# Performance work log

Measured on AMD Instinct MI355X. Metric: run time of the kernel, lower is better.

Reference implementation:

```python
import jax, jax.numpy as jnp
import numpy as np

B, N, D = 16, 2048, 1024
H, DH = 8, 64
I = H * DH            # 512
L = 64                # num_latents
DEPTH = 6
FF = 4 * D


def setup_inputs() -> dict:
    key = jax.random.key(0)
    ks = jax.random.split(key, 8)
    s = 0.02  # weight scale to keep activations well-conditioned
    return {
        "x": jax.random.normal(ks[0], (B, N, D), jnp.float32),
        "mask": jax.random.randint(ks[1], (B, N), 0, 2, jnp.int32),
        "latents": jax.random.normal(ks[2], (L, D), jnp.float32),
        "ln_m_w": jnp.ones((DEPTH, D), jnp.float32),
        "ln_m_b": jnp.zeros((DEPTH, D), jnp.float32),
        "ln_l_w": jnp.ones((DEPTH, D), jnp.float32),
        "ln_l_b": jnp.zeros((DEPTH, D), jnp.float32),
        "Wq": jax.random.normal(ks[3], (DEPTH, D, I), jnp.float32) * s,
        "Wkv": jax.random.normal(ks[4], (DEPTH, D, 2 * I), jnp.float32) * s,
        "Wo": jax.random.normal(ks[5], (DEPTH, I, D), jnp.float32) * s,
        "ff_ln_w": jnp.ones((DEPTH, D), jnp.float32),
        "ff_ln_b": jnp.zeros((DEPTH, D), jnp.float32),
        "W1": jax.random.normal(ks[6], (DEPTH, D, FF), jnp.float32) * s,
        "W2": jax.random.normal(ks[7], (DEPTH, FF, D), jnp.float32) * s,
        "norm_w": jnp.ones((D,), jnp.float32),
        "norm_b": jnp.zeros((D,), jnp.float32),
    }


def _ln(x, w, b, eps=1e-5):
    mu = x.mean(-1, keepdims=True)
    var = ((x - mu) ** 2).mean(-1, keepdims=True)
    return (x - mu) * jax.lax.rsqrt(var + eps) * w + b


def reference(x, mask, latents, ln_m_w, ln_m_b, ln_l_w, ln_l_b,
              Wq, Wkv, Wo, ff_ln_w, ff_ln_b, W1, W2, norm_w, norm_b):
    b, n, d = x.shape
    Lq = latents.shape[0]
    depth = Wq.shape[0]
    h = H
    dh = Wq.shape[-1] // h
    scale = dh ** -0.5

    x4 = x[:, None]  # b 1 n d  (t = 1 media frame)
    lat = jnp.broadcast_to(latents, (b, 1, Lq, d)).astype(x.dtype)
    # mask==1 means masked-out; latents (L zeros) are always attendable
    fmask = jnp.concatenate([mask, jnp.zeros((b, Lq), mask.dtype)], axis=-1)
    mbool = (fmask == 1)[:, None, None, None, :]  # b 1 1 1 S -> broadcast to b t h i S

    for i in range(depth):
        xn = _ln(x4, ln_m_w[i], ln_m_b[i])
        lnl = _ln(lat, ln_l_w[i], ln_l_b[i])
        q = (lnl @ Wq[i]).reshape(b, 1, Lq, h, dh)
        kv = jnp.concatenate([xn, lnl], axis=-2) @ Wkv[i]  # b 1 S 2I
        k, v = jnp.split(kv, 2, axis=-1)
        S = k.shape[-2]
        k = k.reshape(b, 1, S, h, dh)
        v = v.reshape(b, 1, S, h, dh)
        sim = jnp.einsum('btihd,btjhd->bthij', q, k) * scale
        sim = jnp.where(mbool, -jnp.inf, sim)
        sim = sim - jax.lax.stop_gradient(sim.max(axis=-1, keepdims=True))
        attn = jax.nn.softmax(sim, axis=-1)
        out = jnp.einsum('bthij,btjhd->btihd', attn, v).reshape(b, 1, Lq, h * dh)
        lat = out @ Wo[i] + lat
        hf = jax.nn.gelu(_ln(lat, ff_ln_w[i], ff_ln_b[i]) @ W1[i], approximate=False)
        lat = hf @ W2[i] + lat
    return _ln(lat, norm_w, norm_b)
```

## Files before the change

### kernel.cpp

```cpp
#include <hip/hip_runtime.h>

typedef unsigned short u16;
typedef unsigned int u32;
typedef __attribute__((ext_vector_type(8))) short short8;
typedef __attribute__((ext_vector_type(4))) float f4;

#define DEV static __device__ __forceinline__

constexpr int BB = 16, NN = 2048, DD = 1024, HH = 8, DHD = 64, II = 512, LL = 64, DEPTHC = 6, FFC = 4096;

DEV u16 f2bf(float f) {
  union { float f; u32 u; } v; v.f = f;
  u32 r = v.u + 0x7FFFu + ((v.u >> 16) & 1u);
  return (u16)(r >> 16);
}

DEV u32 pack2(float lo, float hi) {
  return (u32)f2bf(lo) | ((u32)f2bf(hi) << 16);
}

typedef const u32 __attribute__((address_space(1)))* gas_p;
typedef u32 __attribute__((address_space(3)))* las_p;
DEV void gl_lds16(const void* g, void* l) {
  __builtin_amdgcn_global_load_lds((gas_p)g, (las_p)l, 16, 0, 0);
}

__global__ __launch_bounds__(256) void maskscan_k(const int* __restrict__ mask,
    int* __restrict__ idx, int* __restrict__ cnt) {
  int b = blockIdx.x, tid = threadIdx.x;
  int lane = tid & 63, wv = tid >> 6;
  const int* mrow = mask + (size_t)b * NN;
  int base = tid * 8;
  int keep[8]; int local = 0;
  #pragma unroll
  for (int j = 0; j < 8; j++) { keep[j] = (mrow[base + j] == 0); local += keep[j]; }
  int incl = local;
  #pragma unroll
  for (int off = 1; off < 64; off <<= 1) {
    int v = __shfl_up(incl, off, 64);
    if (lane >= off) incl += v;
  }
  __shared__ int wsum[4];
  if (lane == 63) wsum[wv] = incl;
  __syncthreads();
  int wbase = 0;
  for (int w = 0; w < wv; w++) wbase += wsum[w];
  int pos = wbase + incl - local;
  #pragma unroll
  for (int j = 0; j < 8; j++) if (keep[j]) idx[(size_t)b * NN + pos++] = base + j;
  if (tid == 255) cnt[b] = wbase + incl;
}

__global__ __launch_bounds__(256) void ln_gather_k(const float* __restrict__ x,
    const int* __restrict__ idx, const int* __restrict__ cnt, u16* __restrict__ xcomp) {
  int b = blockIdx.y, j = blockIdx.x, tid = threadIdx.x;
  int c = cnt[b];
  if (j >= ((c + 127) & ~127)) return;
  ushort4* orow = (ushort4*)(xcomp + ((size_t)b * NN + j) * DD);
  if (j >= c) { orow[tid] = make_ushort4(0, 0, 0, 0); return; }
  int src = idx[(size_t)b * NN + j];
  const float4* rp = (const float4*)(x + ((size_t)b * NN + src) * DD);
  float4 v = rp[tid];
  float s = v.x + v.y + v.z + v.w;
  float s2 = v.x*v.x + v.y*v.y + v.z*v.z + v.w*v.w;
  #pragma unroll
  for (int off = 32; off >= 1; off >>= 1) {
    s  += __shfl_xor(s, off, 64);
    s2 += __shfl_xor(s2, off, 64);
  }
  __shared__ float red[8];
  int wv = tid >> 6;
  if ((tid & 63) == 0) { red[wv] = s; red[4 + wv] = s2; }
  __syncthreads();
  s  = red[0] + red[1] + red[2] + red[3];
  s2 = red[4] + red[5] + red[6] + red[7];
  float mu = s * (1.f / DD);
  float var = s2 * (1.f / DD) - mu * mu;
  float rstd = rsqrtf(var + 1e-5f);
  orow[tid] = make_ushort4(f2bf((v.x - mu) * rstd), f2bf((v.y - mu) * rstd),
                           f2bf((v.z - mu) * rstd), f2bf((v.w - mu) * rstd));
}

template<bool OUTF32>
__global__ __launch_bounds__(256) void ln_rows_k(const float* __restrict__ in,
    const float* __restrict__ w, const float* __restrict__ bias, void* __restrict__ out) {
  int row = blockIdx.x;
  int tid = threadIdx.x;
  const float4* rp = (const float4*)(in + (size_t)row * DD);
  float4 x = rp[tid];
  float s = x.x + x.y + x.z + x.w;
  float s2 = x.x*x.x + x.y*x.y + x.z*x.z + x.w*x.w;
  #pragma unroll
  for (int off = 32; off >= 1; off >>= 1) {
    s  += __shfl_xor(s, off, 64);
    s2 += __shfl_xor(s2, off, 64);
  }
  __shared__ float red[8];
  int wv = tid >> 6;
  if ((tid & 63) == 0) { red[wv] = s; red[4 + wv] = s2; }
  __syncthreads();
  s  = red[0] + red[1] + red[2] + red[3];
  s2 = red[4] + red[5] + red[6] + red[7];
  float mu = s * (1.f / DD);
  float var = s2 * (1.f / DD) - mu * mu;
  float rstd = rsqrtf(var + 1e-5f);
  float y[4] = {x.x, x.y, x.z, x.w};
  int col = tid * 4;
  #pragma unroll
  for (int j = 0; j < 4; j++)
    y[j] = (y[j] - mu) * rstd * w[col + j] + bias[col + j];
  if (OUTF32) {
    float4 o = {y[0], y[1], y[2], y[3]};
    ((float4*)out)[(size_t)row * (DD/4) + tid] = o;
  } else {
    ushort4 o = make_ushort4(f2bf(y[0]), f2bf(y[1]), f2bf(y[2]), f2bf(y[3]));
    ((ushort4*)out)[(size_t)row * (DD/4) + tid] = o;
  }
}

__global__ __launch_bounds__(256) void lat_init_k(const float* __restrict__ latents, float* __restrict__ lat) {
  int idx = blockIdx.x * 256 + threadIdx.x;
  ((float4*)lat)[idx] = ((const float4*)latents)[idx & (LL * DD / 4 - 1)];
}

__global__ void zero_k(float* __restrict__ p, int n) {
  int i = blockIdx.x * 256 + threadIdx.x;
  if (i < n) p[i] = 0.f;
}

__global__ __launch_bounds__(256) void transpall_k(const float* __restrict__ WqA, const float* __restrict__ WkvA,
    const float* __restrict__ WoA, const float* __restrict__ W1A, const float* __restrict__ W2A,
    const float* __restrict__ lnwA, const float* __restrict__ lnbA,
    u16* __restrict__ WqkvTA, u16* __restrict__ WkvTfA, u16* __restrict__ WoTA,
    u16* __restrict__ W1TA, u16* __restrict__ W2TA, float* __restrict__ biaskvA) {
  __shared__ float t[64][65];
  int gid = blockIdx.x;
  int depth = gid / 2560;
  int id = gid % 2560;
  const float* in; u16* o1; int R, C, c0, r0;
  bool iskv = false;
  if (id < 128)       { in = WqA  + (size_t)depth*1024*512;  R = 1024; C = 512;  int l = id;        c0 = (l & 7) * 64;  r0 = (l >> 3) * 64; o1 = WqkvTA + (size_t)depth*1536*1024; }
  else if (id < 384)  { in = WkvA + (size_t)depth*1024*1024; R = 1024; C = 1024; int l = id - 128;  c0 = (l & 15) * 64; r0 = (l >> 4) * 64; o1 = WqkvTA + (size_t)depth*1536*1024 + 512*1024; iskv = true; }
  else if (id < 512)  { in = WoA  + (size_t)depth*512*1024;  R = 512;  C = 1024; int l = id - 384;  c0 = (l & 15) * 64; r0 = (l >> 4) * 64; o1 = WoTA + (size_t)depth*1024*512; }
  else if (id < 1536) { in = W1A  + (size_t)depth*1024*4096; R = 1024; C = 4096; int l = id - 512;  c0 = (l & 63) * 64; r0 = (l >> 6) * 64; o1 = W1TA + (size_t)depth*4096*1024; }
  else                { in = W2A  + (size_t)depth*4096*1024; R = 4096; C = 1024; int l = id - 1536; c0 = (l & 15) * 64; r0 = (l >> 4) * 64; o1 = W2TA + (size_t)depth*1024*4096; }
  int tid = threadIdx.x;
  int lr = tid >> 4, lc4 = (tid & 15) * 4;
  #pragma unroll
  for (int p = 0; p < 4; p++) {
    int row = p * 16 + lr;
    float4 v = *(const float4*)&in[(size_t)(r0 + row) * C + c0 + lc4];
    t[row][lc4] = v.x; t[row][lc4+1] = v.y; t[row][lc4+2] = v.z; t[row][lc4+3] = v.w;
  }
  int oc = tid >> 3;
  int rg = tid & 7;
  float lw[8], lb[8];
  if (iskv) {
    const float* lnw = lnwA + depth * 1024;
    const float* lnb = lnbA + depth * 1024;
    int rbase = r0 + rg * 8;
    float4 w0 = *(const float4*)&lnw[rbase];
    float4 w1 = *(const float4*)&lnw[rbase + 4];
    float4 b0 = *(const float4*)&lnb[rbase];
    float4 b1 = *(const float4*)&lnb[rbase + 4];
    lw[0]=w0.x; lw[1]=w0.y; lw[2]=w0.z; lw[3]=w0.w; lw[4]=w1.x; lw[5]=w1.y; lw[6]=w1.z; lw[7]=w1.w;
    lb[0]=b0.x; lb[1]=b0.y; lb[2]=b0.z; lb[3]=b0.w; lb[4]=b1.x; lb[5]=b1.y; lb[6]=b1.z; lb[7]=b1.w;
  }
  __syncthreads();
  #pragma unroll
  for (int p = 0; p < 2; p++) {
    int c = p * 32 + oc;
    float v[8];
    #pragma unroll
    for (int k = 0; k < 8; k++) v[k] = t[rg * 8 + k][c];
    int4 o;
    o.x = (int)pack2(v[0], v[1]); o.y = (int)pack2(v[2], v[3]);
    o.z = (int)pack2(v[4], v[5]); o.w = (int)pack2(v[6], v[7]);
    *(int4*)&o1[(size_t)(c0 + c) * R + r0 + rg * 8] = o;
    if (iskv) {
      u16* WkvTf = WkvTfA + (size_t)depth*1024*1024;
      int4 of;
      of.x = (int)pack2(v[0]*lw[0], v[1]*lw[1]); of.y = (int)pack2(v[2]*lw[2], v[3]*lw[3]);
      of.z = (int)pack2(v[4]*lw[4], v[5]*lw[5]); of.w = (int)pack2(v[6]*lw[6], v[7]*lw[7]);
      *(int4*)&WkvTf[(size_t)(c0 + c) * 1024 + r0 + rg * 8] = of;
      float partial = 0.f;
      #pragma unroll
      for (int k = 0; k < 8; k++) partial += lb[k] * v[k];
      partial += __shfl_xor(partial, 1, 64);
      partial += __shfl_xor(partial, 2, 64);
      partial += __shfl_xor(partial, 4, 64);
      if (rg == 0) atomicAdd(&biaskvA[depth*1024 + c0 + c], partial);
    }
  }
}

__global__ __launch_bounds__(256) void gemm_fused_k(
    const u16* __restrict__ xcomp, const u16* __restrict__ WkvTf,
    u16* __restrict__ kvk, u16* __restrict__ vT,
    const float* __restrict__ bias, const int* __restrict__ cnt,
    const u16* __restrict__ lnl, const u16* __restrict__ WqkvT, u16* __restrict__ qkv) {
  __shared__ __align__(16) u16 As[128 * 32];
  __shared__ __align__(16) u16 Bs[128 * 32];
  int id = blockIdx.x;
  int tid = threadIdx.x;
  int wv = tid >> 6, lane = tid & 63;
  const u16 *A, *B;
  int m0, n0, batch = 0, ml = 0;
  bool iskv;
  if (id < 2048) {
    int xg = id & 7, t = id >> 3;
    int mtile = xg * 32 + (t >> 3);
    n0 = (t & 7) * 128;
    batch = mtile >> 4;
    ml = (mtile & 15) * 128;
    if (ml >= cnt[batch]) return;
    m0 = batch * NN + ml;
    A = xcomp; B = WkvTf; iskv = true;
  } else {
    int l = id - 2048;
    m0 = (l / 12) * 128; n0 = (l % 12) * 128;
    A = lnl; B = WqkvT; iskv = false;
  }
  const int K = 1024;
  int srow = wv * 16 + (lane >> 2);
  int scol = (lane & 3) * 8;
  const u16* gA0 = A + (size_t)(m0 + srow) * K + scol;
  const u16* gA1 = A + (size_t)(m0 + 64 + srow) * K + scol;
  const u16* gB0 = B + (size_t)(n0 + srow) * K + scol;
  const u16* gB1 = B + (size_t)(n0 + 64 + srow) * K + scol;
  u16* lA0 = &As[srow * 32 + scol];
  u16* lA1 = &As[(64 + srow) * 32 + scol];
  u16* lB0 = &Bs[srow * 32 + scol];
  u16* lB1 = &Bs[(64 + srow) * 32 + scol];
  int wm = (wv & 1) * 64, wn = (wv >> 1) * 64;
  int fr = lane & 15, fq = (lane >> 4) * 8;
  f4 acc[4][4];
  #pragma unroll
  for (int mi = 0; mi < 4; mi++)
    #pragma unroll
    for (int ni = 0; ni < 4; ni++) acc[mi][ni] = f4{0.f, 0.f, 0.f, 0.f};

  for (int k0 = 0; k0 < K; k0 += 32) {
    gl_lds16(gA0 + k0, lA0);
    gl_lds16(gA1 + k0, lA1);
    gl_lds16(gB0 + k0, lB0);
    gl_lds16(gB1 + k0, lB1);
    __syncthreads();
    short8 af[4], bfr[4];
    #pragma unroll
    for (int mi = 0; mi < 4; mi++)
      af[mi] = *(const short8*)&As[(wm + mi*16 + fr) * 32 + fq];
    #pragma unroll
    for (int ni = 0; ni < 4; ni++)
      bfr[ni] = *(const short8*)&Bs[(wn + ni*16 + fr) * 32 + fq];
    #pragma unroll
    for (int mi = 0; mi < 4; mi++)
      #pragma unroll
      for (int ni = 0; ni < 4; ni++)
        acc[mi][ni] = __builtin_amdgcn_mfma_f32_16x16x32_bf16(af[mi], bfr[ni], acc[mi][ni], 0, 0, 0);
    __syncthreads();
  }
  int er = (lane >> 4) * 4;
  int ec = lane & 15;
  if (iskv) {
    #pragma unroll
    for (int mi = 0; mi < 4; mi++) {
      int rbase = wm + mi*16 + er;
      #pragma unroll
      for (int ni = 0; ni < 4; ni++) {
        int col = n0 + wn + ni*16 + ec;
        float bv = bias[col];
        if (col < 512) {
          #pragma unroll
          for (int r = 0; r < 4; r++)
            kvk[(size_t)(m0 + rbase + r) * 512 + col] = f2bf(acc[mi][ni][r] + bv);
        } else {
          int d = col - 512;
          int hh = d >> 6, dl = d & 63;
          ushort4 o4;
          o4.x = f2bf(acc[mi][ni][0] + bv);
          o4.y = f2bf(acc[mi][ni][1] + bv);
          o4.z = f2bf(acc[mi][ni][2] + bv);
          o4.w = f2bf(acc[mi][ni][3] + bv);
          *(ushort4*)(vT + ((size_t)((batch * 8 + hh) * 64 + dl)) * NN + (ml + rbase)) = o4;
        }
      }
    }
  } else {
    #pragma unroll
    for (int mi = 0; mi < 4; mi++)
      #pragma unroll
      for (int ni = 0; ni < 4; ni++) {
        int col = n0 + wn + ni*16 + ec;
        #pragma unroll
        for (int r = 0; r < 4; r++) {
          int row = m0 + wm + mi*16 + er + r;
          qkv[(size_t)row * 1536 + col] = f2bf(acc[mi][ni][r]);
        }
      }
  }
}

__global__ __launch_bounds__(256) void gemm_gelu_k(const u16* __restrict__ A, const u16* __restrict__ Bm,
    u16* __restrict__ C, int M, int N, int K) {
  __shared__ __align__(16) u16 As[128 * 32];
  __shared__ __align__(16) u16 Bs[64 * 32];
  int tid = threadIdx.x;
  int wv = tid >> 6, lane = tid & 63;
  int m0 = blockIdx.y * 128, n0 = blockIdx.x * 64;
  int srow = wv * 16 + (lane >> 2);
  int scol = (lane & 3) * 8;
  const u16* gA0 = A + (size_t)(m0 + srow) * K + scol;
  const u16* gA1 = A + (size_t)(m0 + 64 + srow) * K + scol;
  const u16* gB0 = Bm + (size_t)(n0 + srow) * K + scol;
  u16* lA0 = &As[srow * 32 + scol];
  u16* lA1 = &As[(64 + srow) * 32 + scol];
  u16* lB0 = &Bs[srow * 32 + scol];
  int wm = (wv & 1) * 64, wn = (wv >> 1) * 32;
  int fr = lane & 15, fq = (lane >> 4) * 8;
  f4 acc[4][2];
  #pragma unroll
  for (int mi = 0; mi < 4; mi++)
    #pragma unroll
    for (int ni = 0; ni < 2; ni++) acc[mi][ni] = f4{0.f, 0.f, 0.f, 0.f};

  for (int k0 = 0; k0 < K; k0 += 32) {
    gl_lds16(gA0 + k0, lA0);
    gl_lds16(gA1 + k0, lA1);
    gl_lds16(gB0 + k0, lB0);
    __syncthreads();
    short8 af[4], bfr[2];
    #pragma unroll
    for (int mi = 0; mi < 4; mi++)
      af[mi] = *(const short8*)&As[(wm + mi*16 + fr) * 32 + fq];
    #pragma unroll
    for (int ni = 0; ni < 2; ni++)
      bfr[ni] = *(const short8*)&Bs[(wn + ni*16 + fr) * 32 + fq];
    #pragma unroll
    for (int mi = 0; mi < 4; mi++)
      #pragma unroll
      for (int ni = 0; ni < 2; ni++)
        acc[mi][ni] = __builtin_amdgcn_mfma_f32_16x16x32_bf16(af[mi], bfr[ni], acc[mi][ni], 0, 0, 0);
    __syncthreads();
  }
  int er = (lane >> 4) * 4;
  int ec = lane & 15;
  #pragma unroll
  for (int mi = 0; mi < 4; mi++)
    #pragma unroll
    for (int ni = 0; ni < 2; ni++) {
      int col = n0 + wn + ni*16 + ec;
      #pragma unroll
      for (int r = 0; r < 4; r++) {
        int row = m0 + wm + mi*16 + er + r;
        float v = acc[mi][ni][r];
        v = 0.5f * v * (1.f + erff(v * 0.70710678118654752f));
        C[(size_t)row * N + col] = f2bf(v);
      }
    }
}

__global__ __launch_bounds__(256) void gemmsk_k(const u16* __restrict__ A, const u16* __restrict__ Bm,
    float* __restrict__ C, int M, int N, int K, int Kc) {
  __shared__ __align__(16) u16 As[128 * 32];
  __shared__ __align__(16) u16 Bs[64 * 32];
  int tid = threadIdx.x;
  int wv = tid >> 6, lane = tid & 63;
  int m0 = blockIdx.y * 128, n0 = blockIdx.x * 64;
  int kb = blockIdx.z * Kc;
  int srow = wv * 16 + (lane >> 2);
  int scol = (lane & 3) * 8;
  const u16* gA0 = A + (size_t)(m0 + srow) * K + kb + scol;
  const u16* gA1 = A + (size_t)(m0 + 64 + srow) * K + kb + scol;
  const u16* gB0 = Bm + (size_t)(n0 + srow) * K + kb + scol;
  u16* lA0 = &As[srow * 32 + scol];
  u16* lA1 = &As[(64 + srow) * 32 + scol];
  u16* lB0 = &Bs[srow * 32 + scol];
  int wm = (wv & 1) * 64, wn = (wv >> 1) * 32;
  int fr = lane & 15, fq = (lane >> 4) * 8;
  f4 acc[4][2];
  #pragma unroll
  for (int mi = 0; mi < 4; mi++)
    #pragma unroll
    for (int ni = 0; ni < 2; ni++) acc[mi][ni] = f4{0.f, 0.f, 0.f, 0.f};

  for (int k0 = 0; k0 < Kc; k0 += 32) {
    gl_lds16(gA0 + k0, lA0);
    gl_lds16(gA1 + k0, lA1);
    gl_lds16(gB0 + k0, lB0);
    __syncthreads();
    short8 af[4], bfr[2];
    #pragma unroll
    for (int mi = 0; mi < 4; mi++)
      af[mi] = *(const short8*)&As[(wm + mi*16 + fr) * 32 + fq];
    #pragma unroll
    for (int ni = 0; ni < 2; ni++)
      bfr[ni] = *(const short8*)&Bs[(wn + ni*16 + fr) * 32 + fq];
    #pragma unroll
    for (int mi = 0; mi < 4; mi++)
      #pragma unroll
      for (int ni = 0; ni < 2; ni++)
        acc[mi][ni] = __builtin_amdgcn_mfma_f32_16x16x32_bf16(af[mi], bfr[ni], acc[mi][ni], 0, 0, 0);
    __syncthreads();
  }
  int er = (lane >> 4) * 4;
  int ec = lane & 15;
  #pragma unroll
  for (int mi = 0; mi < 4; mi++)
    #pragma unroll
    for (int ni = 0; ni < 2; ni++) {
      int col = n0 + wn + ni*16 + ec;
      #pragma unroll
      for (int r = 0; r < 4; r++) {
        int row = m0 + wm + mi*16 + er + r;
        atomicAdd(&C[(size_t)row * N + col], acc[mi][ni][r]);
      }
    }
}

__global__ __launch_bounds__(256) void attn_part_k(const u16* __restrict__ qkv,
    const u16* __restrict__ kvk, const u16* __restrict__ vT, const int* __restrict__ cnt,
    float* __restrict__ opart, float* __restrict__ mlpart) {
  int id = blockIdx.x;
  int b = id >> 6;
  int h = (id >> 3) & 7;
  int part = id & 7;
  int tid = threadIdx.x;
  int wv = tid >> 6, lane = tid & 63;
  int fr = lane & 15, fq8 = (lane >> 4) * 8;
  int c = cnt[b];
  int nt = (c + 63) >> 6;
  int T = nt + 1;
  int t0 = (T * part) >> 3;
  int t1 = (T * (part + 1)) >> 3;

  __shared__ __align__(16) u16 ks[64 * 88];
  __shared__ __align__(16) u16 vs[64 * 88];
  __shared__ __align__(16) u16 ps[4][16 * 88];
  __shared__ float smask[64];

  const u16* qp = qkv + (size_t)(b * LL + wv * 16 + fr) * 1536 + h * DHD;
  short8 aq0 = *(const short8*)(qp + fq8);
  short8 aq1 = *(const short8*)(qp + 32 + fq8);

  float m_i[4], l_i[4];
  f4 o[4];
  #pragma unroll
  for (int r = 0; r < 4; r++) { m_i[r] = -1e30f; l_i[r] = 0.f; }
  #pragma unroll
  for (int dt = 0; dt < 4; dt++) o[dt] = f4{0.f, 0.f, 0.f, 0.f};

  const float scale = 0.125f;

  for (int t = t0; t < t1; t++) {
    bool isLat = (t == nt);
    __syncthreads();
    if (isLat) {
      const u16* src = qkv + (size_t)(b * LL) * 1536 + 512 + h * DHD;
      #pragma unroll
      for (int it = 0; it < 2; it++) {
        int cid = it * 256 + tid;
        int kr = cid >> 3, c8 = (cid & 7) * 8;
        int4 kvv = *(const int4*)(src + (size_t)kr * 1536 + c8);
        *(int4*)&ks[kr * 88 + c8] = kvv;
        int4 vvv = *(const int4*)(src + 512 + (size_t)kr * 1536 + c8);
        const u16* ve = (const u16*)&vvv;
        #pragma unroll
        for (int j = 0; j < 8; j++) vs[(c8 + j) * 88 + kr] = ve[j];
      }
    } else {
      const u16* ksrc = kvk + (size_t)(b * NN + t * 64) * 512 + h * DHD;
      const u16* vsrc = vT + (size_t)((b * 8 + h) * 64) * NN + t * 64;
      #pragma unroll
      for (int it = 0; it < 2; it++) {
        int cid = it * 256 + tid;
        int kr = cid >> 3, c8 = (cid & 7) * 8;
        *(int4*)&ks[kr * 88 + c8] = *(const int4*)(ksrc + (size_t)kr * 512 + c8);
        *(int4*)&vs[kr * 88 + c8] = *(const int4*)(vsrc + (size_t)kr * NN + c8);
      }
    }
    if (tid < 64)
      smask[tid] = (isLat || (t * 64 + tid < c)) ? 0.f : -1e30f;
    __syncthreads();

    f4 sim[4];
    #pragma unroll
    for (int ct = 0; ct < 4; ct++) {
      short8 b0 = *(const short8*)&ks[(ct*16 + fr) * 88 + fq8];
      short8 b1 = *(const short8*)&ks[(ct*16 + fr) * 88 + 32 + fq8];
      f4 s = f4{0.f, 0.f, 0.f, 0.f};
      s = __builtin_amdgcn_mfma_f32_16x16x32_bf16(aq0, b0, s, 0, 0, 0);
      s = __builtin_amdgcn_mfma_f32_16x16x32_bf16(aq1, b1, s, 0, 0, 0);
      float mk = smask[ct*16 + fr];
      #pragma unroll
      for (int r = 0; r < 4; r++) s[r] = s[r] * scale + mk;
      sim[ct] = s;
    }
    float mnew[4], alpha[4], p[4][4];
    #pragma unroll
    for (int r = 0; r < 4; r++) {
      float mx = fmaxf(fmaxf(sim[0][r], sim[1][r]), fmaxf(sim[2][r], sim[3][r]));
      #pragma unroll
      for (int off = 8; off >= 1; off >>= 1) mx = fmaxf(mx, __shfl_xor(mx, off, 16));
      mnew[r] = fmaxf(m_i[r], mx);
      alpha[r] = __expf(m_i[r] - mnew[r]);
      m_i[r] = mnew[r];
      float ssum = 0.f;
      #pragma unroll
      for (int ct = 0; ct < 4; ct++) { float e = __expf(sim[ct][r] - mnew[r]); p[ct][r] = e; ssum += e; }
      #pragma unroll
      for (int off = 8; off >= 1; off >>= 1) ssum += __shfl_xor(ssum, off, 16);
      l_i[r] = l_i[r] * alpha[r] + ssum;
    }
    #pragma unroll
    for (int ct = 0; ct < 4; ct++)
      #pragma unroll
      for (int r = 0; r < 4; r++)
        ps[wv][((lane>>4)*4 + r) * 88 + ct*16 + fr] = f2bf(p[ct][r]);
    #pragma unroll
    for (int dt = 0; dt < 4; dt++)
      #pragma unroll
      for (int r = 0; r < 4; r++) o[dt][r] *= alpha[r];
    short8 pa0 = *(const short8*)&ps[wv][fr * 88 + fq8];
    short8 pa1 = *(const short8*)&ps[wv][fr * 88 + 32 + fq8];
    #pragma unroll
    for (int dt = 0; dt < 4; dt++) {
      short8 bv0 = *(const short8*)&vs[(dt*16 + fr) * 88 + fq8];
      short8 bv1 = *(const short8*)&vs[(dt*16 + fr) * 88 + 32 + fq8];
      o[dt] = __builtin_amdgcn_mfma_f32_16x16x32_bf16(pa0, bv0, o[dt], 0, 0, 0);
      o[dt] = __builtin_amdgcn_mfma_f32_16x16x32_bf16(pa1, bv1, o[dt], 0, 0, 0);
    }
  }
  #pragma unroll
  for (int dt = 0; dt < 4; dt++)
    #pragma unroll
    for (int r = 0; r < 4; r++) {
      int row = wv * 16 + (lane>>4)*4 + r;
      int col = dt*16 + fr;
      opart[((size_t)id * 64 + row) * 64 + col] = o[dt][r];
    }
  if (fr == 0) {
    #pragma unroll
    for (int r = 0; r < 4; r++) {
      int row = wv * 16 + (lane>>4)*4 + r;
      mlpart[id * 128 + row * 2]     = m_i[r];
      mlpart[id * 128 + row * 2 + 1] = l_i[r];
    }
  }
}

__global__ __launch_bounds__(256) void attn_comb_k(const float* __restrict__ opart,
    const float* __restrict__ mlpart, u16* __restrict__ out) {
  int bh = blockIdx.x;
  int b = bh >> 3, h = bh & 7;
  int tid = threadIdx.x;
  int row = tid >> 2;
  int c0 = (tid & 3) * 16;
  float mp[8], lp[8];
  float m = -1e30f;
  #pragma unroll
  for (int p = 0; p < 8; p++) {
    mp[p] = mlpart[(bh * 8 + p) * 128 + row * 2];
    lp[p] = mlpart[(bh * 8 + p) * 128 + row * 2 + 1];
    m = fmaxf(m, mp[p]);
  }
  float a[8]; float L = 0.f;
  #pragma unroll
  for (int p = 0; p < 8; p++) { a[p] = __expf(mp[p] - m); L += lp[p] * a[p]; }
  float rl = 1.f / L;
  u16* op = out + ((size_t)(b * LL + row)) * II + h * DHD + c0;
  #pragma unroll
  for (int j = 0; j < 4; j++) {
    float acc4[4] = {0.f, 0.f, 0.f, 0.f};
    #pragma unroll
    for (int p = 0; p < 8; p++) {
      const float4* pp = (const float4*)(opart + ((size_t)(bh * 8 + p) * 64 + row) * 64 + c0);
      float4 v = pp[j];
      acc4[0] += v.x * a[p]; acc4[1] += v.y * a[p];
      acc4[2] += v.z * a[p]; acc4[3] += v.w * a[p];
    }
    op[j*4 + 0] = f2bf(acc4[0] * rl);
    op[j*4 + 1] = f2bf(acc4[1] * rl);
    op[j*4 + 2] = f2bf(acc4[2] * rl);
    op[j*4 + 3] = f2bf(acc4[3] * rl);
  }
}

extern "C" void kernel_launch(void* const* d_in, const int* in_sizes, int n_in,
                              void* d_out, int out_size, void* d_ws, size_t ws_size,
                              hipStream_t stream) {
  (void)in_sizes; (void)n_in; (void)out_size; (void)ws_size;
  const float* x       = (const float*)d_in[0];
  const int*   mask    = (const int*)d_in[1];
  const float* latents = (const float*)d_in[2];
  const float* ln_m_w  = (const float*)d_in[3];
  const float* ln_m_b  = (const float*)d_in[4];
  const float* ln_l_w  = (const float*)d_in[5];
  const float* ln_l_b  = (const float*)d_in[6];
  const float* Wq      = (const float*)d_in[7];
  const float* Wkv     = (const float*)d_in[8];
  const float* Wo      = (const float*)d_in[9];
  const float* ff_ln_w = (const float*)d_in[10];
  const float* ff_ln_b = (const float*)d_in[11];
  const float* W1      = (const float*)d_in[12];
  const float* W2      = (const float*)d_in[13];
  const float* norm_w  = (const float*)d_in[14];
  const float* norm_b  = (const float*)d_in[15];
  float* out = (float*)d_out;

  char* ws = (char*)d_ws;
  size_t off = 0;
  auto alloc = [&](size_t bytes) -> void* {
    void* p = ws + off; off += (bytes + 255) & ~(size_t)255; return p;
  };
  u16* xcomp = (u16*)alloc((size_t)32768 * 1024 * 2);
  u16* kvk   = (u16*)alloc((size_t)32768 * 512 * 2);
  u16* vT    = (u16*)alloc((size_t)8192 * 2048 * 2);
  int* idxb  = (int*)alloc((size_t)32768 * 4);
  int* cnt   = (int*)alloc(64);
  float* lat = (float*)alloc((size_t)1024 * 1024 * 4);
  u16* lnl   = (u16*)alloc((size_t)1024 * 1024 * 2);
  u16* latn  = (u16*)alloc((size_t)1024 * 1024 * 2);
  u16* qkv   = (u16*)alloc((size_t)1024 * 1536 * 2);
  u16* aout  = (u16*)alloc((size_t)1024 * 512 * 2);
  u16* hf    = (u16*)alloc((size_t)1024 * 4096 * 2);
  float* opart  = (float*)alloc((size_t)1024 * 64 * 64 * 4);
  float* mlpart = (float*)alloc((size_t)1024 * 128 * 4);
  u16* WqkvT = (u16*)alloc((size_t)DEPTHC * 1536 * 1024 * 2);
  u16* WkvTf = (u16*)alloc((size_t)DEPTHC * 1024 * 1024 * 2);
  u16* WoT   = (u16*)alloc((size_t)DEPTHC * 1024 * 512 * 2);
  u16* W1T   = (u16*)alloc((size_t)DEPTHC * 4096 * 1024 * 2);
  u16* W2T   = (u16*)alloc((size_t)DEPTHC * 1024 * 4096 * 2);
  float* biaskv_all = (float*)alloc(DEPTHC * 1024 * 4);

  maskscan_k<<<16, 256, 0, stream>>>(mask, idxb, cnt);
  ln_gather_k<<<dim3(2048, 16), 256, 0, stream>>>(x, idxb, cnt, xcomp);
  lat_init_k<<<1024, 256, 0, stream>>>(latents, lat);
  zero_k<<<24, 256, 0, stream>>>(biaskv_all, DEPTHC * 1024);
  transpall_k<<<DEPTHC * 2560, 256, 0, stream>>>(
      Wq, Wkv, Wo, W1, W2, ln_m_w, ln_m_b,
      WqkvT, WkvTf, WoT, W1T, W2T, biaskv_all);

  for (int i = 0; i < DEPTHC; i++) {
    ln_rows_k<false><<<1024, 256, 0, stream>>>(lat, ln_l_w + i*1024, ln_l_b + i*1024, lnl);
    gemm_fused_k<<<2144, 256, 0, stream>>>(
        xcomp, WkvTf + (size_t)i*1024*1024, kvk, vT, biaskv_all + i*1024, cnt,
        lnl, WqkvT + (size_t)i*1536*1024, qkv);
    attn_part_k<<<1024, 256, 0, stream>>>(qkv, kvk, vT, cnt, opart, mlpart);
    attn_comb_k<<<128, 256, 0, stream>>>(opart, mlpart, aout);
    gemmsk_k<<<dim3(16, 8, 4), 256, 0, stream>>>(aout, WoT + (size_t)i*1024*512, lat, 1024, 1024, 512, 128);
    ln_rows_k<false><<<1024, 256, 0, stream>>>(lat, ff_ln_w + i*1024, ff_ln_b + i*1024, latn);
    gemm_gelu_k<<<dim3(64, 8), 256, 0, stream>>>(latn, W1T + (size_t)i*4096*1024, hf, 1024, 4096, 1024);
    gemmsk_k<<<dim3(16, 8, 4), 256, 0, stream>>>(hf, W2T + (size_t)i*1024*4096, lat, 1024, 1024, 4096, 1024);
  }
  ln_rows_k<true><<<1024, 256, 0, stream>>>(lat, norm_w, norm_b, out);
}
```

Measured before the change: 1.527 ms.

## Split weight transposes, fuse QKVO prep with gather and latent init, halve attention splits

The monolithic weight-transpose kernel is split into two launches for W1 and W2 and one fused kernel. The fused kernel handles the Wq/Wkv/Wo transposes, the masked LayerNorm gather of x, and the latent initialisation in a single grid, which removes separate launches and lets these independent jobs share the device. Separately, the split-K attention now uses 4 partitions per (batch, head) instead of 8. That halves the partial-output traffic and the combine work, in exchange for less parallelism in attn_part_k (512 blocks instead of 1024).

```diff
diff --git a/kernel.cpp b/kernel.cpp
--- a/kernel.cpp
+++ b/kernel.cpp
@@ -51,34 +51,145 @@
   if (tid == 255) cnt[b] = wbase + incl;
 }
 
-__global__ __launch_bounds__(256) void ln_gather_k(const float* __restrict__ x,
-    const int* __restrict__ idx, const int* __restrict__ cnt, u16* __restrict__ xcomp) {
-  int b = blockIdx.y, j = blockIdx.x, tid = threadIdx.x;
-  int c = cnt[b];
-  if (j >= ((c + 127) & ~127)) return;
-  ushort4* orow = (ushort4*)(xcomp + ((size_t)b * NN + j) * DD);
-  if (j >= c) { orow[tid] = make_ushort4(0, 0, 0, 0); return; }
-  int src = idx[(size_t)b * NN + j];
-  const float4* rp = (const float4*)(x + ((size_t)b * NN + src) * DD);
-  float4 v = rp[tid];
-  float s = v.x + v.y + v.z + v.w;
-  float s2 = v.x*v.x + v.y*v.y + v.z*v.z + v.w*v.w;
-  #pragma unroll
-  for (int off = 32; off >= 1; off >>= 1) {
-    s  += __shfl_xor(s, off, 64);
-    s2 += __shfl_xor(s2, off, 64);
-  }
-  __shared__ float red[8];
-  int wv = tid >> 6;
-  if ((tid & 63) == 0) { red[wv] = s; red[4 + wv] = s2; }
+__global__ void zero_k(float* __restrict__ p, int n) {
+  int i = blockIdx.x * 256 + threadIdx.x;
+  if (i < n) p[i] = 0.f;
+}
+
+__global__ __launch_bounds__(256) void transp_w_k(const float* __restrict__ Wa, u16* __restrict__ WTa,
+    int R, int C, int ctLog) {
+  __shared__ float t[64][65];
+  int gid = blockIdx.x;
+  int depth = gid >> 10;
+  int l = gid & 1023;
+  int c0 = (l & ((1 << ctLog) - 1)) << 6;
+  int r0 = (l >> ctLog) << 6;
+  const float* in = Wa + (size_t)depth * 4096 * 1024;
+  u16* o1 = WTa + (size_t)depth * 4096 * 1024;
+  int tid = threadIdx.x;
+  int lr = tid >> 4, lc4 = (tid & 15) * 4;
+  #pragma unroll
+  for (int p = 0; p < 4; p++) {
+    int row = p * 16 + lr;
+    float4 v = *(const float4*)&in[(size_t)(r0 + row) * C + c0 + lc4];
+    t[row][lc4] = v.x; t[row][lc4+1] = v.y; t[row][lc4+2] = v.z; t[row][lc4+3] = v.w;
+  }
   __syncthreads();
-  s  = red[0] + red[1] + red[2] + red[3];
-  s2 = red[4] + red[5] + red[6] + red[7];
-  float mu = s * (1.f / DD);
-  float var = s2 * (1.f / DD) - mu * mu;
-  float rstd = rsqrtf(var + 1e-5f);
-  orow[tid] = make_ushort4(f2bf((v.x - mu) * rstd), f2bf((v.y - mu) * rstd),
-                           f2bf((v.z - mu) * rstd), f2bf((v.w - mu) * rstd));
+  int oc = tid >> 3;
+  int rg = tid & 7;
+  #pragma unroll
+  for (int p = 0; p < 2; p++) {
+    int c = p * 32 + oc;
+    float v[8];
+    #pragma unroll
+    for (int k = 0; k < 8; k++) v[k] = t[rg * 8 + k][c];
+    int4 o;
+    o.x = (int)pack2(v[0], v[1]); o.y = (int)pack2(v[2], v[3]);
+    o.z = (int)pack2(v[4], v[5]); o.w = (int)pack2(v[6], v[7]);
+    *(int4*)&o1[(size_t)(c0 + c) * R + r0 + rg * 8] = o;
+  }
+}
+
+__global__ __launch_bounds__(256) void qkvo_fused_k(
+    const float* __restrict__ WqA, const float* __restrict__ WkvA, const float* __restrict__ WoA,
+    const float* __restrict__ lnwA, const float* __restrict__ lnbA,
+    u16* __restrict__ WqkvTA, u16* __restrict__ WoTA, u16* __restrict__ WkvTfA,
+    float* __restrict__ biaskvA,
+    const float* __restrict__ x, const int* __restrict__ idx, const int* __restrict__ cnt,
+    u16* __restrict__ xcomp, const float* __restrict__ latents, float* __restrict__ lat) {
+  __shared__ float t[64][65];
+  __shared__ float red8[8];
+  int gid = blockIdx.x;
+  int tid = threadIdx.x;
+  if (gid < 3072) {
+    int depth = gid >> 9;
+    int id = gid & 511;
+    const float* in; u16* o1; int R, C, c0, r0;
+    bool iskv = false;
+    if (id < 128)      { in = WqA  + (size_t)depth*1024*512;  R = 1024; C = 512;  int l = id;       c0 = (l & 7) * 64;  r0 = (l >> 3) * 64; o1 = WqkvTA + (size_t)depth*1536*1024; }
+    else if (id < 384) { in = WkvA + (size_t)depth*1024*1024; R = 1024; C = 1024; int l = id - 128; c0 = (l & 15) * 64; r0 = (l >> 4) * 64; o1 = WqkvTA + (size_t)depth*1536*1024 + 512*1024; iskv = true; }
+    else               { in = WoA  + (size_t)depth*512*1024;  R = 512;  C = 1024; int l = id - 384; c0 = (l & 15) * 64; r0 = (l >> 4) * 64; o1 = WoTA + (size_t)depth*1024*512; }
+    int lr = tid >> 4, lc4 = (tid & 15) * 4;
+    #pragma unroll
+    for (int p = 0; p < 4; p++) {
+      int row = p * 16 + lr;
+      float4 v = *(const float4*)&in[(size_t)(r0 + row) * C + c0 + lc4];
+      t[row][lc4] = v.x; t[row][lc4+1] = v.y; t[row][lc4+2] = v.z; t[row][lc4+3] = v.w;
+    }
+    int oc = tid >> 3;
+    int rg = tid & 7;
+    float lw[8], lb[8];
+    if (iskv) {
+      const float* lnw = lnwA + depth * 1024;
+      const float* lnb = lnbA + depth * 1024;
+      int rbase = r0 + rg * 8;
+      float4 w0 = *(const float4*)&lnw[rbase];
+      float4 w1 = *(const float4*)&lnw[rbase + 4];
+      float4 b0 = *(const float4*)&lnb[rbase];
+      float4 b1 = *(const float4*)&lnb[rbase + 4];
+      lw[0]=w0.x; lw[1]=w0.y; lw[2]=w0.z; lw[3]=w0.w; lw[4]=w1.x; lw[5]=w1.y; lw[6]=w1.z; lw[7]=w1.w;
+      lb[0]=b0.x; lb[1]=b0.y; lb[2]=b0.z; lb[3]=b0.w; lb[4]=b1.x; lb[5]=b1.y; lb[6]=b1.z; lb[7]=b1.w;
+    }
+    __syncthreads();
+    #pragma unroll
+    for (int p = 0; p < 2; p++) {
+      int c = p * 32 + oc;
+      float v[8];
+      #pragma unroll
+      for (int k = 0; k < 8; k++) v[k] = t[rg * 8 + k][c];
+      int4 o;
+      o.x = (int)pack2(v[0], v[1]); o.y = (int)pack2(v[2], v[3]);
+      o.z = (int)pack2(v[4], v[5]); o.w = (int)pack2(v[6], v[7]);
+      *(int4*)&o1[(size_t)(c0 + c) * R + r0 + rg * 8] = o;
+      if (iskv) {
+        u16* WkvTf = WkvTfA + (size_t)depth*1024*1024;
+        int4 of;
+        of.x = (int)pack2(v[0]*lw[0], v[1]*lw[1]); of.y = (int)pack2(v[2]*lw[2], v[3]*lw[3]);
+        of.z = (int)pack2(v[4]*lw[4], v[5]*lw[5]); of.w = (int)pack2(v[6]*lw[6], v[7]*lw[7]);
+        *(int4*)&WkvTf[(size_t)(c0 + c) * 1024 + r0 + rg * 8] = of;
+        float partial = 0.f;
+        #pragma unroll
+        for (int k = 0; k < 8; k++) partial += lb[k] * v[k];
+        partial += __shfl_xor(partial, 1, 64);
+        partial += __shfl_xor(partial, 2, 64);
+        partial += __shfl_xor(partial, 4, 64);
+        if (rg == 0) atomicAdd(&biaskvA[depth*1024 + c0 + c], partial);
+      }
+    }
+    return;
+  }
+  gid -= 3072;
+  if (gid < 32768) {
+    int b = gid >> 11, j = gid & 2047;
+    int c = cnt[b];
+    if (j >= ((c + 127) & ~127)) return;
+    ushort4* orow = (ushort4*)(xcomp + ((size_t)b * NN + j) * DD);
+    if (j >= c) { orow[tid] = make_ushort4(0, 0, 0, 0); return; }
+    int src = idx[(size_t)b * NN + j];
+    const float4* rp = (const float4*)(x + ((size_t)b * NN + src) * DD);
+    float4 v = rp[tid];
+    float s = v.x + v.y + v.z + v.w;
+    float s2 = v.x*v.x + v.y*v.y + v.z*v.z + v.w*v.w;
+    #pragma unroll
+    for (int off = 32; off >= 1; off >>= 1) {
+      s  += __shfl_xor(s, off, 64);
+      s2 += __shfl_xor(s2, off, 64);
+    }
+    int wv = tid >> 6;
+    if ((tid & 63) == 0) { red8[wv] = s; red8[4 + wv] = s2; }
+    __syncthreads();
+    s  = red8[0] + red8[1] + red8[2] + red8[3];
+    s2 = red8[4] + red8[5] + red8[6] + red8[7];
+    float mu = s * (1.f / DD);
+    float var = s2 * (1.f / DD) - mu * mu;
+    float rstd = rsqrtf(var + 1e-5f);
+    orow[tid] = make_ushort4(f2bf((v.x - mu) * rstd), f2bf((v.y - mu) * rstd),
+                             f2bf((v.z - mu) * rstd), f2bf((v.w - mu) * rstd));
+    return;
+  }
+  gid -= 32768;
+  int i2 = gid * 256 + tid;
+  ((float4*)lat)[i2] = ((const float4*)latents)[i2 & (LL * DD / 4 - 1)];
 }
 
 template<bool OUTF32>
@@ -115,82 +226,6 @@
   } else {
     ushort4 o = make_ushort4(f2bf(y[0]), f2bf(y[1]), f2bf(y[2]), f2bf(y[3]));
     ((ushort4*)out)[(size_t)row * (DD/4) + tid] = o;
-  }
-}
-
-__global__ __launch_bounds__(256) void lat_init_k(const float* __restrict__ latents, float* __restrict__ lat) {
-  int idx = blockIdx.x * 256 + threadIdx.x;
-  ((float4*)lat)[idx] = ((const float4*)latents)[idx & (LL * DD / 4 - 1)];
-}
-
-__global__ void zero_k(float* __restrict__ p, int n) {
-  int i = blockIdx.x * 256 + threadIdx.x;
-  if (i < n) p[i] = 0.f;
-}
-
-__global__ __launch_bounds__(256) void transpall_k(const float* __restrict__ WqA, const float* __restrict__ WkvA,
-    const float* __restrict__ WoA, const float* __restrict__ W1A, const float* __restrict__ W2A,
-    const float* __restrict__ lnwA, const float* __restrict__ lnbA,
-    u16* __restrict__ WqkvTA, u16* __restrict__ WkvTfA, u16* __restrict__ WoTA,
-    u16* __restrict__ W1TA, u16* __restrict__ W2TA, float* __restrict__ biaskvA) {
-  __shared__ float t[64][65];
-  int gid = blockIdx.x;
-  int depth = gid / 2560;
-  int id = gid % 2560;
-  const float* in; u16* o1; int R, C, c0, r0;
-  bool iskv = false;
-  if (id < 128)       { in = WqA  + (size_t)depth*1024*512;  R = 1024; C = 512;  int l = id;        c0 = (l & 7) * 64;  r0 = (l >> 3) * 64; o1 = WqkvTA + (size_t)depth*1536*1024; }
-  else if (id < 384)  { in = WkvA + (size_t)depth*1024*1024; R = 1024; C = 1024; int l = id - 128;  c0 = (l & 15) * 64; r0 = (l >> 4) * 64; o1 = WqkvTA + (size_t)depth*1536*1024 + 512*1024; iskv = true; }
-  else if (id < 512)  { in = WoA  + (size_t)depth*512*1024;  R = 512;  C = 1024; int l = id - 384;  c0 = (l & 15) * 64; r0 = (l >> 4) * 64; o1 = WoTA + (size_t)depth*1024*512; }
-  else if (id < 1536) { in = W1A  + (size_t)depth*1024*4096; R = 1024; C = 4096; int l = id - 512;  c0 = (l & 63) * 64; r0 = (l >> 6) * 64; o1 = W1TA + (size_t)depth*4096*1024; }
-  else                { in = W2A  + (size_t)depth*4096*1024; R = 4096; C = 1024; int l = id - 1536; c0 = (l & 15) * 64; r0 = (l >> 4) * 64; o1 = W2TA + (size_t)depth*1024*4096; }
-  int tid = threadIdx.x;
-  int lr = tid >> 4, lc4 = (tid & 15) * 4;
-  #pragma unroll
-  for (int p = 0; p < 4; p++) {
-    int row = p * 16 + lr;
-    float4 v = *(const float4*)&in[(size_t)(r0 + row) * C + c0 + lc4];
-    t[row][lc4] = v.x; t[row][lc4+1] = v.y; t[row][lc4+2] = v.z; t[row][lc4+3] = v.w;
-  }
-  int oc = tid >> 3;
-  int rg = tid & 7;
-  float lw[8], lb[8];
-  if (iskv) {
-    const float* lnw = lnwA + depth * 1024;
-    const float* lnb = lnbA + depth * 1024;
-    int rbase = r0 + rg * 8;
-    float4 w0 = *(const float4*)&lnw[rbase];
-    float4 w1 = *(const float4*)&lnw[rbase + 4];
-    float4 b0 = *(const float4*)&lnb[rbase];
-    float4 b1 = *(const float4*)&lnb[rbase + 4];
-    lw[0]=w0.x; lw[1]=w0.y; lw[2]=w0.z; lw[3]=w0.w; lw[4]=w1.x; lw[5]=w1.y; lw[6]=w1.z; lw[7]=w1.w;
-    lb[0]=b0.x; lb[1]=b0.y; lb[2]=b0.z; lb[3]=b0.w; lb[4]=b1.x; lb[5]=b1.y; lb[6]=b1.z; lb[7]=b1.w;
-  }
-  __syncthreads();
-  #pragma unroll
-  for (int p = 0; p < 2; p++) {
-    int c = p * 32 + oc;
-    float v[8];
-    #pragma unroll
-    for (int k = 0; k < 8; k++) v[k] = t[rg * 8 + k][c];
-    int4 o;
-    o.x = (int)pack2(v[0], v[1]); o.y = (int)pack2(v[2], v[3]);
-    o.z = (int)pack2(v[4], v[5]); o.w = (int)pack2(v[6], v[7]);
-    *(int4*)&o1[(size_t)(c0 + c) * R + r0 + rg * 8] = o;
-    if (iskv) {
-      u16* WkvTf = WkvTfA + (size_t)depth*1024*1024;
-      int4 of;
-      of.x = (int)pack2(v[0]*lw[0], v[1]*lw[1]); of.y = (int)pack2(v[2]*lw[2], v[3]*lw[3]);
-      of.z = (int)pack2(v[4]*lw[4], v[5]*lw[5]); of.w = (int)pack2(v[6]*lw[6], v[7]*lw[7]);
-      *(int4*)&WkvTf[(size_t)(c0 + c) * 1024 + r0 + rg * 8] = of;
-      float partial = 0.f;
-      #pragma unroll
-      for (int k = 0; k < 8; k++) partial += lb[k] * v[k];
-      partial += __shfl_xor(partial, 1, 64);
-      partial += __shfl_xor(partial, 2, 64);
-      partial += __shfl_xor(partial, 4, 64);
-      if (rg == 0) atomicAdd(&biaskvA[depth*1024 + c0 + c], partial);
-    }
   }
 }
 
@@ -422,17 +457,17 @@
     const u16* __restrict__ kvk, const u16* __restrict__ vT, const int* __restrict__ cnt,
     float* __restrict__ opart, float* __restrict__ mlpart) {
   int id = blockIdx.x;
-  int b = id >> 6;
-  int h = (id >> 3) & 7;
-  int part = id & 7;
+  int b = id >> 5;
+  int h = (id >> 2) & 7;
+  int part = id & 3;
   int tid = threadIdx.x;
   int wv = tid >> 6, lane = tid & 63;
   int fr = lane & 15, fq8 = (lane >> 4) * 8;
   int c = cnt[b];
   int nt = (c + 63) >> 6;
   int T = nt + 1;
-  int t0 = (T * part) >> 3;
-  int t1 = (T * (part + 1)) >> 3;
+  int t0 = (T * part) >> 2;
+  int t1 = (T * (part + 1)) >> 2;
 
   __shared__ __align__(16) u16 ks[64 * 88];
   __shared__ __align__(16) u16 vs[64 * 88];
@@ -556,25 +591,25 @@
   int tid = threadIdx.x;
   int row = tid >> 2;
   int c0 = (tid & 3) * 16;
-  float mp[8], lp[8];
+  float mp[4], lp[4];
   float m = -1e30f;
   #pragma unroll
-  for (int p = 0; p < 8; p++) {
-    mp[p] = mlpart[(bh * 8 + p) * 128 + row * 2];
-    lp[p] = mlpart[(bh * 8 + p) * 128 + row * 2 + 1];
+  for (int p = 0; p < 4; p++) {
+    mp[p] = mlpart[(bh * 4 + p) * 128 + row * 2];
+    lp[p] = mlpart[(bh * 4 + p) * 128 + row * 2 + 1];
     m = fmaxf(m, mp[p]);
   }
-  float a[8]; float L = 0.f;
-  #pragma unroll
-  for (int p = 0; p < 8; p++) { a[p] = __expf(mp[p] - m); L += lp[p] * a[p]; }
+  float a[4]; float L = 0.f;
+  #pragma unroll
+  for (int p = 0; p < 4; p++) { a[p] = __expf(mp[p] - m); L += lp[p] * a[p]; }
   float rl = 1.f / L;
   u16* op = out + ((size_t)(b * LL + row)) * II + h * DHD + c0;
   #pragma unroll
   for (int j = 0; j < 4; j++) {
     float acc4[4] = {0.f, 0.f, 0.f, 0.f};
     #pragma unroll
-    for (int p = 0; p < 8; p++) {
-      const float4* pp = (const float4*)(opart + ((size_t)(bh * 8 + p) * 64 + row) * 64 + c0);
+    for (int p = 0; p < 4; p++) {
+      const float4* pp = (const float4*)(opart + ((size_t)(bh * 4 + p) * 64 + row) * 64 + c0);
       float4 v = pp[j];
       acc4[0] += v.x * a[p]; acc4[1] += v.y * a[p];
       acc4[2] += v.z * a[p]; acc4[3] += v.w * a[p];
@@ -624,8 +659,8 @@
   u16* qkv   = (u16*)alloc((size_t)1024 * 1536 * 2);
   u16* aout  = (u16*)alloc((size_t)1024 * 512 * 2);
   u16* hf    = (u16*)alloc((size_t)1024 * 4096 * 2);
-  float* opart  = (float*)alloc((size_t)1024 * 64 * 64 * 4);
-  float* mlpart = (float*)alloc((size_t)1024 * 128 * 4);
+  float* opart  = (float*)alloc((size_t)512 * 64 * 64 * 4);
+  float* mlpart = (float*)alloc((size_t)512 * 128 * 4);
   u16* WqkvT = (u16*)alloc((size_t)DEPTHC * 1536 * 1024 * 2);
   u16* WkvTf = (u16*)alloc((size_t)DEPTHC * 1024 * 1024 * 2);
   u16* WoT   = (u16*)alloc((size_t)DEPTHC * 1024 * 512 * 2);
@@ -634,19 +669,20 @@
   float* biaskv_all = (float*)alloc(DEPTHC * 1024 * 4);
 
   maskscan_k<<<16, 256, 0, stream>>>(mask, idxb, cnt);
-  ln_gather_k<<<dim3(2048, 16), 256, 0, stream>>>(x, idxb, cnt, xcomp);
-  lat_init_k<<<1024, 256, 0, stream>>>(latents, lat);
   zero_k<<<24, 256, 0, stream>>>(biaskv_all, DEPTHC * 1024);
-  transpall_k<<<DEPTHC * 2560, 256, 0, stream>>>(
-      Wq, Wkv, Wo, W1, W2, ln_m_w, ln_m_b,
-      WqkvT, WkvTf, WoT, W1T, W2T, biaskv_all);
+  transp_w_k<<<DEPTHC * 1024, 256, 0, stream>>>(W1, W1T, 1024, 4096, 6);
+  transp_w_k<<<DEPTHC * 1024, 256, 0, stream>>>(W2, W2T, 4096, 1024, 4);
+  qkvo_fused_k<<<3072 + 32768 + 1024, 256, 0, stream>>>(
+      Wq, Wkv, Wo, ln_m_w, ln_m_b,
+      WqkvT, WoT, WkvTf, biaskv_all,
+      x, idxb, cnt, xcomp, latents, lat);
 
   for (int i = 0; i < DEPTHC; i++) {
     ln_rows_k<false><<<1024, 256, 0, stream>>>(lat, ln_l_w + i*1024, ln_l_b + i*1024, lnl);
     gemm_fused_k<<<2144, 256, 0, stream>>>(
         xcomp, WkvTf + (size_t)i*1024*1024, kvk, vT, biaskv_all + i*1024, cnt,
         lnl, WqkvT + (size_t)i*1536*1024, qkv);
-    attn_part_k<<<1024, 256, 0, stream>>>(qkv, kvk, vT, cnt, opart, mlpart);
+    attn_part_k<<<512, 256, 0, stream>>>(qkv, kvk, vT, cnt, opart, mlpart);
     attn_comb_k<<<128, 256, 0, stream>>>(opart, mlpart, aout);
     gemmsk_k<<<dim3(16, 8, 4), 256, 0, stream>>>(aout, WoT + (size_t)i*1024*512, lat, 1024, 1024, 512, 128);
     ln_rows_k<false><<<1024, 256, 0, stream>>>(lat, ff_ln_w + i*1024, ff_ln_b + i*1024, latn);
```

Result: faster. 1.459 ms (-4.4%).
